# Kernel optimization log

Hardware: AMD Instinct MI355X
Metric: run time of the kernel (lower is better)

The kernel has to match this reference:

```python
import jax, jax.numpy as jnp
import numpy as np

B, T, N, D, H, NMASK = 8192, 2, 40, 64, 1, 3
EPS = 1e-5


def setup_inputs() -> dict:
    key = jax.random.key(0)
    ks = jax.random.split(key, 12)
    F = T * N * 2 * D  # flattened feature size fed to BatchNorm1d
    return {
        "x": jax.random.normal(ks[0], (B, N, D), jnp.float32),
        "masker": jax.random.uniform(ks[1], (T, NMASK, N, N), jnp.float32, -0.27, 0.27),  # xavier-like
        "ln_gamma": jnp.ones((N,), jnp.float32),
        "ln_beta": jnp.zeros((N,), jnp.float32),
        "gnn_w": jax.random.normal(ks[2], (1, T, H, 2 * D, D), jnp.float32) * 0.05,
        "gnn_b": jax.random.normal(ks[3], (T, H, N, D), jnp.float32) * 0.05,
        "bn_gamma": jnp.ones((H, F), jnp.float32),
        "bn_beta": jnp.zeros((H, F), jnp.float32),
        "bn_mean": jax.random.normal(ks[4], (H, F), jnp.float32) * 0.1,
        "bn_var": jax.random.uniform(ks[5], (H, F), jnp.float32, 0.5, 1.5),
        "gate_w": jax.random.normal(ks[6], (N * D, N), jnp.float32) * 0.02,
        "gate_b": jnp.zeros((N,), jnp.float32),
    }


def reference(x, masker, ln_gamma, ln_beta, gnn_w, gnn_b, bn_gamma, bn_beta, bn_mean, bn_var, gate_w, gate_b):
    b = x.shape[0]
    # broadcast input to towers: (B, T, N, D)
    h = jnp.broadcast_to(x[:, None], (b, T, N, D))
    # adjacency from product of mask matrices: (T, N, N)
    adj = jax.nn.relu(jnp.prod(masker, axis=1))
    mask = (adj != 0).astype(x.dtype)
    # LayerNorm(num_fields) applied on transposed adj == normalize over rows (axis -2)
    mu = adj.mean(axis=-2, keepdims=True)
    var = adj.var(axis=-2, keepdims=True)
    ln = (adj - mu) / jnp.sqrt(var + EPS) * ln_gamma[:, None] + ln_beta[:, None]
    x_masked = ln + (1.0 - mask) * (-1e9) + jnp.eye(N, dtype=x.dtype)
    # softmax over rows (dim=1 of (T,N,N)) then re-mask
    A = jax.nn.softmax(x_masked, axis=1) * mask  # (T, N, N)
    for idx in range(H):
        # nei[b,t,n,d] = sum_m h[b,t,m,d] * A[t,m,n]
        nei = jnp.einsum('btmd,tmn->btnd', h, A)
        hc = jnp.concatenate([h, nei], axis=-1)  # (B,T,N,2D)
        flat = hc.reshape(b, -1)
        flat = (flat - bn_mean[idx]) / jnp.sqrt(bn_var[idx] + EPS) * bn_gamma[idx] + bn_beta[idx]
        hc = flat.reshape(b, T, N, 2 * D)
        # per-tower transform: (B,T,N,2D) x (T,2D,D) -> (B,T,N,D)
        h = jnp.einsum('btnf,tfd->btnd', hc, gnn_w[0, :, idx]) + gnn_b[:, idx]
    # attention pooling over fields
    logits = h.reshape(b, T, N * D) @ gate_w + gate_b  # (B,T,N)
    w = jax.nn.softmax(logits, axis=2)
    return jnp.sum(h * w[..., None], axis=2)  # (B, T, D)
```

## Files before the change

kernel.cpp:

```cpp
#include <hip/hip_runtime.h>
#include <hip/hip_bf16.h>
#include <stdint.h>

typedef float v4f __attribute__((ext_vector_type(4)));
typedef short v8s __attribute__((ext_vector_type(8)));

#define NB 40

__device__ __forceinline__ unsigned short f2b(float f) {
  __hip_bfloat16 h = __float2bfloat16(f);
  unsigned short u;
  __builtin_memcpy(&u, &h, 2);
  return u;
}
__device__ __forceinline__ unsigned pk2(float lo, float hi) {
  __hip_bfloat162 h = __float22bfloat162_rn(make_float2(lo, hi));
  unsigned u;
  __builtin_memcpy(&u, &h, 4);
  return u;
}
__device__ __forceinline__ float b2f16(unsigned short h) {
  return __uint_as_float(((unsigned)h) << 16);
}
__device__ __forceinline__ float blo(unsigned u) { return __uint_as_float(u << 16); }
__device__ __forceinline__ float bhi(unsigned u) { return __uint_as_float(u & 0xFFFF0000u); }


__global__ __launch_bounds__(256) void prep(
    const float* __restrict__ masker,
    const float* __restrict__ ln_gamma, const float* __restrict__ ln_beta,
    const float* __restrict__ gnn_w, const float* __restrict__ gnn_b,
    const float* __restrict__ bn_gamma, const float* __restrict__ bn_beta,
    const float* __restrict__ bn_mean, const float* __restrict__ bn_var,
    const float* __restrict__ gate_w,
    unsigned short* __restrict__ A1pk, unsigned short* __restrict__ W2pk,
    unsigned short* __restrict__ Gpk, float* __restrict__ s1,
    float* __restrict__ sNT, float* __restrict__ bias2T)
{
  const int tid = threadIdx.x;
  if (blockIdx.x == 0) {
    __shared__ float AtL[2 * NB * NB];
    const int w = tid >> 6, lane = tid & 63;
    #pragma unroll 1
    for (int it = 0; it < 20; ++it) {
      const int c = it * 4 + w;
      const int t = c / NB, n = c % NB;
      const int m = lane;
      float adj = 0.f;
      if (m < NB) {
        float p = masker[((t*3+0)*NB+m)*NB+n]
                * masker[((t*3+1)*NB+m)*NB+n]
                * masker[((t*3+2)*NB+m)*NB+n];
        adj = p > 0.f ? p : 0.f;
      }
      float s = adj;
      #pragma unroll
      for (int d = 1; d < 64; d <<= 1) s += __shfl_xor(s, d);
      const float mu = s * (1.f/NB);
      const float dv = (m < NB) ? adj - mu : 0.f;
      float v2 = dv * dv;
      #pragma unroll
      for (int d = 1; d < 64; d <<= 1) v2 += __shfl_xor(v2, d);
      const float inv = rsqrtf(v2 * (1.f/NB) + 1e-5f);
      float val = -3.0e38f;
      if (m < NB) {
        float lnv = dv * inv * ln_gamma[m] + ln_beta[m];
        val = lnv + (adj != 0.f ? 0.f : -1e9f) + (m == n ? 1.f : 0.f);
      }
      float mx = val;
      #pragma unroll
      for (int d = 1; d < 64; d <<= 1) mx = fmaxf(mx, __shfl_xor(mx, d));
      const float e = (m < NB) ? __expf(val - mx) : 0.f;
      float es = e;
      #pragma unroll
      for (int d = 1; d < 64; d <<= 1) es += __shfl_xor(es, d);
      if (m < NB)
        AtL[(t*NB+n)*NB + m] = (adj != 0.f) ? e / es : 0.f;
    }
    __syncthreads();
    for (int e = tid; e < 6144; e += 256) {
      int frag = e >> 9, rem = e & 511, lane2 = rem >> 3, jj = rem & 7;
      int t = frag / 6, r2 = frag % 6, nt = r2 >> 1, ks = r2 & 1;
      int n = nt*16 + (lane2 & 15);
      int m = ks*32 + (lane2 >> 4)*8 + jj;
      A1pk[e] = f2b((n < NB && m < NB) ? AtL[(t*NB+n)*NB+m] : 0.f);
    }
  } else {
    const int gid = (blockIdx.x - 1) * 256 + tid, gsz = 63 * 256;
    for (int e = gid; e < 16384; e += gsz) {
      int frag = e >> 9, rem = e & 511, lane = rem >> 3, jj = rem & 7;
      int t = frag >> 4, ks = (frag >> 2) & 3, dt = frag & 3;
      int f = ks*32 + (lane >> 4)*8 + jj, d = dt*16 + (lane & 15);
      W2pk[e] = f2b(gnn_w[t*8192 + f*64 + d]);
    }
    for (int e = gid; e < 122880; e += gsz) {
      int frag = e >> 9, rem = e & 511, lane = rem >> 3, jj = rem & 7;
      int kt = frag / 3, jt = frag % 3;
      int fl = kt*32 + (lane >> 4)*8 + jj, j = jt*16 + (lane & 15);
      Gpk[e] = f2b(j < NB ? gate_w[fl*NB + j] : 0.f);
    }
    for (int e = gid; e < 5120; e += gsz) {
      int t = e / 2560, n = (e % 2560) / 64, d = e & 63;
      int F = (t*NB + n)*128 + d;
      s1[e] = bn_gamma[F] * rsqrtf(bn_var[F] + 1e-5f);
    }
    for (int e = gid; e < 5120; e += gsz) {
      int t = e / 2560, d = (e % 2560) / 40, n = e % 40;
      int F = (t*NB + n)*128 + 64 + d;
      sNT[e] = bn_gamma[F] * rsqrtf(bn_var[F] + 1e-5f);
    }
    for (int e4 = gid; e4 < 20480; e4 += gsz) {
      int e = e4 >> 2, part = e4 & 3;
      int t = e / 2560, d = (e % 2560) / 40, n = e % 40;
      float acc = (part == 0) ? gnn_b[(t*NB + n)*64 + d] : 0.f;
      int Fb = (t*NB + n)*128;
      int f0 = part * 32;
      for (int f = f0; f < f0 + 32; ++f) {
        float s = bn_gamma[Fb+f] * rsqrtf(bn_var[Fb+f] + 1e-5f);
        float o = bn_beta[Fb+f] - bn_mean[Fb+f] * s;
        acc += o * gnn_w[t*8192 + f*64 + d];
      }
      acc += __shfl_xor(acc, 1);
      acc += __shfl_xor(acc, 2);
      if (part == 0) bias2T[e] = acc;
    }
  }
}

__global__ __launch_bounds__(256) void kernelA(
    const float* __restrict__ x,
    const unsigned short* __restrict__ A1pk, const unsigned short* __restrict__ W2pk,
    const float* __restrict__ s1, const float* __restrict__ sNT,
    const float* __restrict__ bias2T, unsigned short* __restrict__ hLg)
{
  __shared__ __align__(16) unsigned short hc[160 * 136];

  const int tid = threadIdx.x;
  const int lane = tid & 63;
  const int w = tid >> 6;
  const int l = lane & 15, q = lane >> 4;
  const int b0 = blockIdx.x * 4;
  unsigned* hcU = (unsigned*)hc;

  uint4 xr[5];
  #pragma unroll
  for (int it = 0; it < 5; ++it) {
    const int c = it * 256 + tid, row = c >> 3, dp8 = c & 7;
    const float* xp = x + (size_t)b0 * 2560 + row * 64 + dp8 * 8;
    const float4 f0 = *(const float4*)xp;
    const float4 f1 = *(const float4*)(xp + 4);
    xr[it] = make_uint4(pk2(f0.x, f0.y), pk2(f0.z, f0.w),
                        pk2(f1.x, f1.y), pk2(f1.z, f1.w));
  }
  if (tid < 12) hcU[5120 + tid] = 0u;
  #pragma unroll
  for (int it = 0; it < 5; ++it) {
    const int c = it * 256 + tid, row = c >> 3, dp8 = c & 7;
    const int bq = row / NB, n = row - bq * NB;
    unsigned short* base = hc + (bq * 64 + dp8 * 8) * NB + n;
    const unsigned uu0 = xr[it].x, uu1 = xr[it].y, uu2 = xr[it].z, uu3 = xr[it].w;
    base[0*NB] = (unsigned short)(uu0 & 0xFFFF);
    base[1*NB] = (unsigned short)(uu0 >> 16);
    base[2*NB] = (unsigned short)(uu1 & 0xFFFF);
    base[3*NB] = (unsigned short)(uu1 >> 16);
    base[4*NB] = (unsigned short)(uu2 & 0xFFFF);
    base[5*NB] = (unsigned short)(uu2 >> 16);
    base[6*NB] = (unsigned short)(uu3 & 0xFFFF);
    base[7*NB] = (unsigned short)(uu3 >> 16);
  }
  __syncthreads();
  v8s b1[4][2];
  #pragma unroll
  for (int i = 0; i < 4; ++i)
    #pragma unroll
    for (int ks = 0; ks < 2; ++ks)
      b1[i][ks] = *(const v8s*)(hc + ((w * 4 + i) * 16 + l) * NB + ks * 32 + q * 8);
  __syncthreads();

  #pragma unroll
  for (int t = 0; t < 2; ++t) {
    if (t) __syncthreads();

    v8s a1[3][2], w2[4];
    #pragma unroll
    for (int nt = 0; nt < 3; ++nt)
      #pragma unroll
      for (int ks = 0; ks < 2; ++ks)
        a1[nt][ks] = *(const v8s*)(A1pk + (((t*3 + nt)*2 + ks) << 9) + lane*8);
    #pragma unroll
    for (int ks = 0; ks < 4; ++ks)
      w2[ks] = *(const v8s*)(W2pk + (((t*4 + ks)*4 + w) << 9) + lane*8);

    #pragma unroll
    for (int it = 0; it < 5; ++it) {
      const int c = it*256 + tid;
      const int row = c >> 3, dp8 = c & 7;
      const uint4 xv = xr[it];
      const int n = row % NB;
      const float4 sA = *(const float4*)(s1 + (t*NB + n)*64 + dp8*8);
      const float4 sB = *(const float4*)(s1 + (t*NB + n)*64 + dp8*8 + 4);
      uint4 p;
      p.x = pk2(blo(xv.x)*sA.x, bhi(xv.x)*sA.y);
      p.y = pk2(blo(xv.y)*sA.z, bhi(xv.y)*sA.w);
      p.z = pk2(blo(xv.z)*sB.x, bhi(xv.z)*sB.y);
      p.w = pk2(blo(xv.w)*sB.z, bhi(xv.w)*sB.w);
      *(uint4*)(hcU + row*68 + dp8*4) = p;
    }
    #pragma unroll
    for (int i = 0; i < 4; ++i) {
      const int R = (w*4+i)*16 + l;
      const int bb = R >> 6, d = R & 63;
      #pragma unroll
      for (int nt = 0; nt < 3; ++nt) {
        v4f acc = {0.f, 0.f, 0.f, 0.f};
        acc = __builtin_amdgcn_mfma_f32_16x16x32_bf16(a1[nt][0], b1[i][0], acc, 0, 0, 0);
        acc = __builtin_amdgcn_mfma_f32_16x16x32_bf16(a1[nt][1], b1[i][1], acc, 0, 0, 0);
        const float4 sv = *(const float4*)(sNT + (t*64+d)*40 + nt*16 + q*4);
        #pragma unroll
        for (int r = 0; r < 4; ++r) {
          int n = nt*16 + q*4 + r;
          if (n < NB) hc[(bb*NB + n)*136 + 64 + d] = f2b(acc[r]*sv[r]);
        }
      }
    }
    __syncthreads();
    #pragma unroll
    for (int mt = 0; mt < 10; ++mt) {
      v4f acc = {0.f, 0.f, 0.f, 0.f};
      #pragma unroll
      for (int ks = 0; ks < 4; ++ks) {
        v8s af = *(const v8s*)(hc + (mt*16 + l)*136 + ks*32 + q*8);
        acc = __builtin_amdgcn_mfma_f32_16x16x32_bf16(af, w2[ks], acc, 0, 0, 0);
      }
      const int d = w*16 + l;
      const int G = mt*16 + q*4;
      const int bb = G / NB, n0 = G - bb*NB;
      const float4 bv = *(const float4*)(bias2T + (t*64+d)*40 + n0);
      unsigned short* hp = hLg + ((size_t)(b0 + bb)*2 + t)*2560 + n0*64 + d;
      hp[0*64] = f2b(acc[0] + bv.x);
      hp[1*64] = f2b(acc[1] + bv.y);
      hp[2*64] = f2b(acc[2] + bv.z);
      hp[3*64] = f2b(acc[3] + bv.w);
    }
  }
}

__global__ __launch_bounds__(512) void kernelB(
    const unsigned short* __restrict__ hLg, const unsigned short* __restrict__ Gpk,
    const float* __restrict__ gate_b, float* __restrict__ out)
{
  __shared__ float pj[8 * 48 * 17];
  __shared__ float wgt[16 * NB];

  const int tid = threadIdx.x;
  const int w = tid >> 6, lane = tid & 63;
  const int l = lane & 15, q = lane >> 4;
  const int b0 = blockIdx.x * 16;

  v4f ac[2][3];
  #pragma unroll
  for (int t = 0; t < 2; ++t)
    #pragma unroll
    for (int jt = 0; jt < 3; ++jt)
      ac[t][jt] = (v4f){0.f, 0.f, 0.f, 0.f};

  const unsigned short* hb = hLg + (size_t)(b0 + l) * 2 * 2560 + q * 8;
  int kt = w;
  v8s g0 = *(const v8s*)(Gpk + ((kt*3+0) << 9) + lane*8);
  v8s g1 = *(const v8s*)(Gpk + ((kt*3+1) << 9) + lane*8);
  v8s g2 = *(const v8s*)(Gpk + ((kt*3+2) << 9) + lane*8);
  v8s bf0 = *(const v8s*)(hb + kt*32);
  v8s bf1 = *(const v8s*)(hb + 2560 + kt*32);
  #pragma unroll
  for (int i = 0; i < 10; ++i) {
    const int ktn = kt + 8;
    v8s ng0, ng1, ng2, nbf0, nbf1;
    if (i < 9) {
      ng0  = *(const v8s*)(Gpk + ((ktn*3+0) << 9) + lane*8);
      ng1  = *(const v8s*)(Gpk + ((ktn*3+1) << 9) + lane*8);
      ng2  = *(const v8s*)(Gpk + ((ktn*3+2) << 9) + lane*8);
      nbf0 = *(const v8s*)(hb + ktn*32);
      nbf1 = *(const v8s*)(hb + 2560 + ktn*32);
    }
    ac[0][0] = __builtin_amdgcn_mfma_f32_16x16x32_bf16(g0, bf0, ac[0][0], 0, 0, 0);
    ac[0][1] = __builtin_amdgcn_mfma_f32_16x16x32_bf16(g1, bf0, ac[0][1], 0, 0, 0);
    ac[0][2] = __builtin_amdgcn_mfma_f32_16x16x32_bf16(g2, bf0, ac[0][2], 0, 0, 0);
    ac[1][0] = __builtin_amdgcn_mfma_f32_16x16x32_bf16(g0, bf1, ac[1][0], 0, 0, 0);
    ac[1][1] = __builtin_amdgcn_mfma_f32_16x16x32_bf16(g1, bf1, ac[1][1], 0, 0, 0);
    ac[1][2] = __builtin_amdgcn_mfma_f32_16x16x32_bf16(g2, bf1, ac[1][2], 0, 0, 0);
    g0 = ng0; g1 = ng1; g2 = ng2; bf0 = nbf0; bf1 = nbf1;
    kt = ktn;
  }

  #pragma unroll
  for (int t = 0; t < 2; ++t) {
    if (t) __syncthreads();
    #pragma unroll
    for (int jt = 0; jt < 3; ++jt)
      #pragma unroll
      for (int r = 0; r < 4; ++r)
        pj[(w*48 + jt*16 + q*4 + r)*17 + l] = ac[t][jt][r];
    __syncthreads();
    #pragma unroll
    for (int hb2 = 0; hb2 < 2; ++hb2) {
      const int b = w*2 + hb2;
      float v = -3.0e38f;
      if (lane < NB) {
        v = gate_b[lane];
        #pragma unroll
        for (int w8 = 0; w8 < 8; ++w8) v += pj[(w8*48 + lane)*17 + b];
      }
      float mx = v;
      #pragma unroll
      for (int m = 1; m < 64; m <<= 1) mx = fmaxf(mx, __shfl_xor(mx, m));
      const float e = (lane < NB) ? __expf(v - mx) : 0.f;
      float es = e;
      #pragma unroll
      for (int m = 1; m < 64; m <<= 1) es += __shfl_xor(es, m);
      if (lane < NB) wgt[b*NB + lane] = e / es;
    }
    __syncthreads();
    #pragma unroll
    for (int hb2 = 0; hb2 < 2; ++hb2) {
      const int b = w*2 + hb2;
      const unsigned short* hp = hLg + ((size_t)(b0 + b)*2 + t)*2560 + lane;
      float a = 0.f;
      #pragma unroll 8
      for (int n = 0; n < NB; ++n)
        a += b2f16(hp[n*64]) * wgt[b*NB + n];
      out[((size_t)(b0 + b)*2 + t)*64 + lane] = a;
    }
  }
}

extern "C" void kernel_launch(void* const* d_in, const int* in_sizes, int n_in,
                              void* d_out, int out_size, void* d_ws, size_t ws_size,
                              hipStream_t stream) {
  const float* x        = (const float*)d_in[0];
  const float* masker   = (const float*)d_in[1];
  const float* ln_gamma = (const float*)d_in[2];
  const float* ln_beta  = (const float*)d_in[3];
  const float* gnn_w    = (const float*)d_in[4];
  const float* gnn_b    = (const float*)d_in[5];
  const float* bn_gamma = (const float*)d_in[6];
  const float* bn_beta  = (const float*)d_in[7];
  const float* bn_mean  = (const float*)d_in[8];
  const float* bn_var   = (const float*)d_in[9];
  const float* gate_w   = (const float*)d_in[10];
  const float* gate_b   = (const float*)d_in[11];
  float* out = (float*)d_out;

  char* ws = (char*)d_ws;
  unsigned short* A1pk   = (unsigned short*)(ws + 0);
  unsigned short* W2pk   = (unsigned short*)(ws + 12288);
  unsigned short* Gpk    = (unsigned short*)(ws + 45056);
  float*          s1     = (float*)(ws + 290816);
  float*          sNT    = (float*)(ws + 311296);
  float*          bias2T = (float*)(ws + 331904);
  unsigned short* hLg    = (unsigned short*)(ws + 352384);

  prep<<<64, 256, 0, stream>>>(masker, ln_gamma, ln_beta, gnn_w, gnn_b,
                               bn_gamma, bn_beta, bn_mean, bn_var, gate_w,
                               A1pk, W2pk, Gpk, s1, sNT, bias2T);
  kernelA<<<2048, 256, 0, stream>>>(x, A1pk, W2pk, s1, sNT, bias2T, hLg);
  kernelB<<<512, 512, 0, stream>>>(hLg, Gpk, gate_b, out);
}
```

Before: 244.9 us.

## Give each wave its own batch element and store intermediate h transposed

kernelA now assigns one batch element per wave and keeps per-wave LDS tiles, which removes the block-wide barriers and the shared staging of all four batch elements. The intermediate h is written transposed (d-major, n-minor) with packed 8-byte stores, and the gate weight packing is permuted to match. kernelB's final weighted sum then reads 16-byte vectors along n instead of strided scalars, and both towers are finalized after a single sync. The cost is more LDS per block, per-wave reloads of the W2 fragments, and scattered 2-byte transposed LDS writes of x.

New measurement: 271.3 us. 10.8% more time.

```diff
diff --git a/kernel.cpp b/kernel.cpp
--- a/kernel.cpp
+++ b/kernel.cpp
@@ -4,6 +4,7 @@
 
 typedef float v4f __attribute__((ext_vector_type(4)));
 typedef short v8s __attribute__((ext_vector_type(8)));
+typedef union { v8s v; unsigned u[4]; } v8u;
 
 #define NB 40
 
@@ -96,8 +97,10 @@
     for (int e = gid; e < 122880; e += gsz) {
       int frag = e >> 9, rem = e & 511, lane = rem >> 3, jj = rem & 7;
       int kt = frag / 3, jt = frag % 3;
-      int fl = kt*32 + (lane >> 4)*8 + jj, j = jt*16 + (lane & 15);
-      Gpk[e] = f2b(j < NB ? gate_w[fl*NB + j] : 0.f);
+      int flp = kt*32 + (lane >> 4)*8 + jj;
+      int dd = flp / 40, nn = flp - dd*40;
+      int j = jt*16 + (lane & 15);
+      Gpk[e] = f2b(j < NB ? gate_w[(nn*64 + dd)*NB + j] : 0.f);
     }
     for (int e = gid; e < 5120; e += gsz) {
       int t = e / 2560, n = (e % 2560) / 64, d = e & 63;
@@ -133,114 +136,123 @@
     const float* __restrict__ s1, const float* __restrict__ sNT,
     const float* __restrict__ bias2T, unsigned short* __restrict__ hLg)
 {
-  __shared__ __align__(16) unsigned short hc[160 * 136];
+  __shared__ __align__(16) unsigned short sh[4*5760 + 576];
 
   const int tid = threadIdx.x;
   const int lane = tid & 63;
   const int w = tid >> 6;
-  const int l = lane & 15, q = lane >> 4;
-  const int b0 = blockIdx.x * 4;
-  unsigned* hcU = (unsigned*)hc;
-
-  uint4 xr[5];
-  #pragma unroll
-  for (int it = 0; it < 5; ++it) {
-    const int c = it * 256 + tid, row = c >> 3, dp8 = c & 7;
-    const float* xp = x + (size_t)b0 * 2560 + row * 64 + dp8 * 8;
-    const float4 f0 = *(const float4*)xp;
-    const float4 f1 = *(const float4*)(xp + 4);
-    xr[it] = make_uint4(pk2(f0.x, f0.y), pk2(f0.z, f0.w),
-                        pk2(f1.x, f1.y), pk2(f1.z, f1.w));
-  }
-  if (tid < 12) hcU[5120 + tid] = 0u;
-  #pragma unroll
-  for (int it = 0; it < 5; ++it) {
-    const int c = it * 256 + tid, row = c >> 3, dp8 = c & 7;
-    const int bq = row / NB, n = row - bq * NB;
-    unsigned short* base = hc + (bq * 64 + dp8 * 8) * NB + n;
-    const unsigned uu0 = xr[it].x, uu1 = xr[it].y, uu2 = xr[it].z, uu3 = xr[it].w;
-    base[0*NB] = (unsigned short)(uu0 & 0xFFFF);
-    base[1*NB] = (unsigned short)(uu0 >> 16);
-    base[2*NB] = (unsigned short)(uu1 & 0xFFFF);
-    base[3*NB] = (unsigned short)(uu1 >> 16);
-    base[4*NB] = (unsigned short)(uu2 & 0xFFFF);
-    base[5*NB] = (unsigned short)(uu2 >> 16);
-    base[6*NB] = (unsigned short)(uu3 & 0xFFFF);
-    base[7*NB] = (unsigned short)(uu3 >> 16);
-  }
-  __syncthreads();
+  const int l15 = lane & 15, q = lane >> 4;
+  const int b = blockIdx.x * 4 + w;
+
+  unsigned short* Uw  = sh + w * 5760;
+  unsigned short* Vw  = Uw + 2880;
+  unsigned short* xTw = Vw;
+
+  const float* xb = x + (size_t)b * 2560;
   v8s b1[4][2];
-  #pragma unroll
-  for (int i = 0; i < 4; ++i)
-    #pragma unroll
-    for (int ks = 0; ks < 2; ++ks)
-      b1[i][ks] = *(const v8s*)(hc + ((w * 4 + i) * 16 + l) * NB + ks * 32 + q * 8);
-  __syncthreads();
-
-  #pragma unroll
+
+  #pragma unroll 1
   for (int t = 0; t < 2; ++t) {
-    if (t) __syncthreads();
-
-    v8s a1[3][2], w2[4];
+    #pragma unroll
+    for (int it = 0; it < 5; ++it) {
+      const int n  = it*8 + (lane >> 3);
+      const int f0 = (lane & 7) * 8;
+      const float* xp = xb + n*64 + f0;
+      const float4 fA = *(const float4*)xp;
+      const float4 fB = *(const float4*)(xp + 4);
+      const float* sp = s1 + (t*NB + n)*64 + f0;
+      const float4 sA = *(const float4*)sp;
+      const float4 sB = *(const float4*)(sp + 4);
+      uint4 p;
+      p.x = pk2(fA.x*sA.x, fA.y*sA.y);
+      p.y = pk2(fA.z*sA.z, fA.w*sA.w);
+      p.z = pk2(fB.x*sB.x, fB.y*sB.y);
+      p.w = pk2(fB.z*sB.z, fB.w*sB.w);
+      *(uint4*)(Uw + n*72 + f0) = p;
+      if (t == 0) {
+        xTw[(f0+0)*42 + n] = f2b(fA.x);
+        xTw[(f0+1)*42 + n] = f2b(fA.y);
+        xTw[(f0+2)*42 + n] = f2b(fA.z);
+        xTw[(f0+3)*42 + n] = f2b(fA.w);
+        xTw[(f0+4)*42 + n] = f2b(fB.x);
+        xTw[(f0+5)*42 + n] = f2b(fB.y);
+        xTw[(f0+6)*42 + n] = f2b(fB.z);
+        xTw[(f0+7)*42 + n] = f2b(fB.w);
+      }
+    }
+    if (t == 0) {
+      #pragma unroll
+      for (int dt = 0; dt < 4; ++dt) {
+        const int r = dt*16 + l15;
+        const unsigned* p0 = (const unsigned*)(xTw + r*42 + q*8);
+        v8u u0;
+        u0.u[0] = p0[0]; u0.u[1] = p0[1]; u0.u[2] = p0[2]; u0.u[3] = p0[3];
+        b1[dt][0] = u0.v;
+        v8s bk1 = {0,0,0,0,0,0,0,0};
+        if (q == 0) {
+          const unsigned* p1 = (const unsigned*)(xTw + r*42 + 32);
+          v8u u1;
+          u1.u[0] = p1[0]; u1.u[1] = p1[1]; u1.u[2] = p1[2]; u1.u[3] = p1[3];
+          bk1 = u1.v;
+        }
+        b1[dt][1] = bk1;
+      }
+    }
+    v8s a1[3][2];
     #pragma unroll
     for (int nt = 0; nt < 3; ++nt)
       #pragma unroll
       for (int ks = 0; ks < 2; ++ks)
         a1[nt][ks] = *(const v8s*)(A1pk + (((t*3 + nt)*2 + ks) << 9) + lane*8);
     #pragma unroll
-    for (int ks = 0; ks < 4; ++ks)
-      w2[ks] = *(const v8s*)(W2pk + (((t*4 + ks)*4 + w) << 9) + lane*8);
-
-    #pragma unroll
-    for (int it = 0; it < 5; ++it) {
-      const int c = it*256 + tid;
-      const int row = c >> 3, dp8 = c & 7;
-      const uint4 xv = xr[it];
-      const int n = row % NB;
-      const float4 sA = *(const float4*)(s1 + (t*NB + n)*64 + dp8*8);
-      const float4 sB = *(const float4*)(s1 + (t*NB + n)*64 + dp8*8 + 4);
-      uint4 p;
-      p.x = pk2(blo(xv.x)*sA.x, bhi(xv.x)*sA.y);
-      p.y = pk2(blo(xv.y)*sA.z, bhi(xv.y)*sA.w);
-      p.z = pk2(blo(xv.z)*sB.x, bhi(xv.z)*sB.y);
-      p.w = pk2(blo(xv.w)*sB.z, bhi(xv.w)*sB.w);
-      *(uint4*)(hcU + row*68 + dp8*4) = p;
-    }
-    #pragma unroll
-    for (int i = 0; i < 4; ++i) {
-      const int R = (w*4+i)*16 + l;
-      const int bb = R >> 6, d = R & 63;
-      #pragma unroll
-      for (int nt = 0; nt < 3; ++nt) {
+    for (int nt = 0; nt < 3; ++nt) {
+      #pragma unroll
+      for (int dt = 0; dt < 4; ++dt) {
         v4f acc = {0.f, 0.f, 0.f, 0.f};
-        acc = __builtin_amdgcn_mfma_f32_16x16x32_bf16(a1[nt][0], b1[i][0], acc, 0, 0, 0);
-        acc = __builtin_amdgcn_mfma_f32_16x16x32_bf16(a1[nt][1], b1[i][1], acc, 0, 0, 0);
-        const float4 sv = *(const float4*)(sNT + (t*64+d)*40 + nt*16 + q*4);
+        acc = __builtin_amdgcn_mfma_f32_16x16x32_bf16(a1[nt][0], b1[dt][0], acc, 0, 0, 0);
+        acc = __builtin_amdgcn_mfma_f32_16x16x32_bf16(a1[nt][1], b1[dt][1], acc, 0, 0, 0);
+        const int d = dt*16 + l15;
+        const float4 sv = *(const float4*)(sNT + (t*64 + d)*40 + nt*16 + q*4);
         #pragma unroll
         for (int r = 0; r < 4; ++r) {
-          int n = nt*16 + q*4 + r;
-          if (n < NB) hc[(bb*NB + n)*136 + 64 + d] = f2b(acc[r]*sv[r]);
+          const int n = nt*16 + q*4 + r;
+          if (n < NB) Vw[n*72 + d] = f2b(acc[r]*sv[r]);
         }
       }
     }
-    __syncthreads();
-    #pragma unroll
-    for (int mt = 0; mt < 10; ++mt) {
-      v4f acc = {0.f, 0.f, 0.f, 0.f};
+    v8s af[3][4];
+    #pragma unroll
+    for (int nt = 0; nt < 3; ++nt) {
+      const unsigned short* rowU = Uw + (nt*16 + l15)*72;
+      const unsigned short* rowV = Vw + (nt*16 + l15)*72;
+      af[nt][0] = *(const v8s*)(rowU + q*8);
+      af[nt][1] = *(const v8s*)(rowU + 32 + q*8);
+      af[nt][2] = *(const v8s*)(rowV + q*8);
+      af[nt][3] = *(const v8s*)(rowV + 32 + q*8);
+    }
+    unsigned short* hLb = hLg + ((size_t)b*2 + t)*2560;
+    #pragma unroll
+    for (int dt = 0; dt < 4; ++dt) {
+      v4f a2[3] = {{0,0,0,0},{0,0,0,0},{0,0,0,0}};
       #pragma unroll
       for (int ks = 0; ks < 4; ++ks) {
-        v8s af = *(const v8s*)(hc + (mt*16 + l)*136 + ks*32 + q*8);
-        acc = __builtin_amdgcn_mfma_f32_16x16x32_bf16(af, w2[ks], acc, 0, 0, 0);
-      }
-      const int d = w*16 + l;
-      const int G = mt*16 + q*4;
-      const int bb = G / NB, n0 = G - bb*NB;
-      const float4 bv = *(const float4*)(bias2T + (t*64+d)*40 + n0);
-      unsigned short* hp = hLg + ((size_t)(b0 + bb)*2 + t)*2560 + n0*64 + d;
-      hp[0*64] = f2b(acc[0] + bv.x);
-      hp[1*64] = f2b(acc[1] + bv.y);
-      hp[2*64] = f2b(acc[2] + bv.z);
-      hp[3*64] = f2b(acc[3] + bv.w);
+        const v8s w2k = *(const v8s*)(W2pk + ((t*16 + ks*4 + dt) << 9) + lane*8);
+        #pragma unroll
+        for (int nt = 0; nt < 3; ++nt)
+          a2[nt] = __builtin_amdgcn_mfma_f32_16x16x32_bf16(af[nt][ks], w2k, a2[nt], 0, 0, 0);
+      }
+      const int d = dt*16 + l15;
+      #pragma unroll
+      for (int nt = 0; nt < 3; ++nt) {
+        const int n0 = nt*16 + q*4;
+        if (n0 < NB) {
+          const float4 bv = *(const float4*)(bias2T + (t*64 + d)*40 + n0);
+          uint2 pr;
+          pr.x = pk2(a2[nt][0] + bv.x, a2[nt][1] + bv.y);
+          pr.y = pk2(a2[nt][2] + bv.z, a2[nt][3] + bv.w);
+          *(uint2*)(hLb + d*40 + n0) = pr;
+        }
+      }
     }
   }
 }
@@ -250,7 +262,7 @@
     const float* __restrict__ gate_b, float* __restrict__ out)
 {
   __shared__ float pj[8 * 48 * 17];
-  __shared__ float wgt[16 * NB];
+  __shared__ float wgt[2 * 16 * NB];
 
   const int tid = threadIdx.x;
   const int w = tid >> 6, lane = tid & 63;
@@ -303,12 +315,12 @@
     __syncthreads();
     #pragma unroll
     for (int hb2 = 0; hb2 < 2; ++hb2) {
-      const int b = w*2 + hb2;
+      const int bb = w*2 + hb2;
       float v = -3.0e38f;
       if (lane < NB) {
         v = gate_b[lane];
         #pragma unroll
-        for (int w8 = 0; w8 < 8; ++w8) v += pj[(w8*48 + lane)*17 + b];
+        for (int w8 = 0; w8 < 8; ++w8) v += pj[(w8*48 + lane)*17 + bb];
       }
       float mx = v;
       #pragma unroll
@@ -317,19 +329,26 @@
       float es = e;
       #pragma unroll
       for (int m = 1; m < 64; m <<= 1) es += __shfl_xor(es, m);
-      if (lane < NB) wgt[b*NB + lane] = e / es;
-    }
-    __syncthreads();
-    #pragma unroll
-    for (int hb2 = 0; hb2 < 2; ++hb2) {
-      const int b = w*2 + hb2;
-      const unsigned short* hp = hLg + ((size_t)(b0 + b)*2 + t)*2560 + lane;
-      float a = 0.f;
-      #pragma unroll 8
-      for (int n = 0; n < NB; ++n)
-        a += b2f16(hp[n*64]) * wgt[b*NB + n];
-      out[((size_t)(b0 + b)*2 + t)*64 + lane] = a;
-    }
+      if (lane < NB) wgt[(t*16 + bb)*NB + lane] = e / es;
+    }
+  }
+  __syncthreads();
+  {
+    const int bb = tid >> 5, t = (tid >> 4) & 1, d0 = (tid & 15) * 4;
+    const uint4* hp4 = (const uint4*)(hLg + ((size_t)(b0 + bb)*2 + t)*2560 + d0*40);
+    const float* wb = wgt + (t*16 + bb)*NB;
+    float s[4] = {0.f, 0.f, 0.f, 0.f};
+    #pragma unroll
+    for (int k = 0; k < 20; ++k) {
+      const uint4 rr = hp4[k];
+      const int e0 = k*8;
+      s[(e0+0)/40] += blo(rr.x)*wb[(e0+0)%40]; s[(e0+1)/40] += bhi(rr.x)*wb[(e0+1)%40];
+      s[(e0+2)/40] += blo(rr.y)*wb[(e0+2)%40]; s[(e0+3)/40] += bhi(rr.y)*wb[(e0+3)%40];
+      s[(e0+4)/40] += blo(rr.z)*wb[(e0+4)%40]; s[(e0+5)/40] += bhi(rr.z)*wb[(e0+5)%40];
+      s[(e0+6)/40] += blo(rr.w)*wb[(e0+6)%40]; s[(e0+7)/40] += bhi(rr.w)*wb[(e0+7)%40];
+    }
+    float4 ov = make_float4(s[0], s[1], s[2], s[3]);
+    *(float4*)(out + ((size_t)(b0 + bb)*2 + t)*64 + d0) = ov;
   }
 }
 
@@ -357,7 +376,7 @@
   float*          s1     = (float*)(ws + 290816);
   float*          sNT    = (float*)(ws + 311296);
   float*          bias2T = (float*)(ws + 331904);
-  unsigned short* hLg    = (unsigned short*)(ws + 352384);
+  unsigned short* hLg    = (unsigned short*)(ws + 352512);
 
   prep<<<64, 256, 0, stream>>>(masker, ln_gamma, ln_beta, gnn_w, gnn_b,
                                bn_gamma, bn_beta, bn_mean, bn_var, gate_w,
```
